# Kernel tuning notes

Hardware: AMD Instinct MI355X
Metric: run time of the kernel (lower is better)

The kernel has to match this reference:

```python
import jax, jax.numpy as jnp
import numpy as np

N_NODES = 50000
N_EDGES = 640000
D_IN = 128
HIDDEN = 128
OUT = 64


def sage_conv(x, edge_index, W_l, b_l, W_r):
    # PyG SAGEConv (mean aggr): out = lin_l(mean_j x_j) + lin_r(x_i)
    src, dst = edge_index[0], edge_index[1]
    msgs = x[src]                                             # [E, d] gather
    agg = jax.ops.segment_sum(msgs, dst, num_segments=x.shape[0])
    cnt = jax.ops.segment_sum(jnp.ones((edge_index.shape[1],), x.dtype), dst,
                              num_segments=x.shape[0])
    mean = agg / jnp.maximum(cnt, 1.0)[:, None]
    return mean @ W_l.T + b_l + x @ W_r.T


def setup_inputs() -> dict:
    key = jax.random.key(0)
    ks = jax.random.split(key, 8)
    s = lambda d: 1.0 / np.sqrt(d)
    x = jax.random.normal(ks[0], (N_NODES, D_IN), dtype=jnp.float32)
    edge_index = jax.random.randint(ks[1], (2, N_EDGES), 0, N_NODES, dtype=jnp.int64)
    return {
        "x": x,
        "edge_index": edge_index,
        "W1_l": jax.random.normal(ks[2], (HIDDEN, D_IN), jnp.float32) * s(D_IN),
        "b1_l": jnp.zeros((HIDDEN,), jnp.float32),
        "W1_r": jax.random.normal(ks[3], (HIDDEN, D_IN), jnp.float32) * s(D_IN),
        "W2_l": jax.random.normal(ks[4], (HIDDEN, HIDDEN), jnp.float32) * s(HIDDEN),
        "b2_l": jnp.zeros((HIDDEN,), jnp.float32),
        "W2_r": jax.random.normal(ks[5], (HIDDEN, HIDDEN), jnp.float32) * s(HIDDEN),
        "W3": jax.random.normal(ks[6], (OUT, HIDDEN), jnp.float32) * s(HIDDEN),
        "b3": jnp.zeros((OUT,), jnp.float32),
    }


def reference(x, edge_index, W1_l, b1_l, W1_r, W2_l, b2_l, W2_r, W3, b3):
    h = jax.nn.relu(sage_conv(x, edge_index, W1_l, b1_l, W1_r))
    h = jax.nn.relu(sage_conv(h, edge_index, W2_l, b2_l, W2_r))
    return h @ W3.T + b3
```

## Files before the change

kernel.cpp:

```cpp
#include <hip/hip_runtime.h>
#include <hip/hip_fp16.h>


typedef _Float16 f16x8 __attribute__((ext_vector_type(8)));
typedef float floatx4 __attribute__((ext_vector_type(4)));
typedef float floatx2 __attribute__((ext_vector_type(2)));

__device__ __forceinline__ unsigned short f2h(float f) {
    __half h = __float2half_rn(f);
    union { __half h; unsigned short s; } c; c.h = h; return c.s;
}
__device__ __forceinline__ __half2 u2h(unsigned u) {
    union { unsigned u; __half2 h; } c; c.u = u; return c.h;
}
__device__ __forceinline__ unsigned h2u(__half2 h) {
    union { __half2 h; unsigned u; } c; c.h = h; return c.u;
}
__device__ __forceinline__ __half2 shx(__half2 v, int m) {
    return u2h((unsigned)__shfl_xor((int)h2u(v), m, 64));
}
__device__ __forceinline__ ushort4 cvt4h(float4 v) {
    ushort4 o;
    o.x = f2h(v.x); o.y = f2h(v.y); o.z = f2h(v.z); o.w = f2h(v.w);
    return o;
}
__device__ __forceinline__ unsigned char f2fp8(float v) {
    return (unsigned char)(__builtin_amdgcn_cvt_pk_fp8_f32(v, v, 0, false) & 0xff);
}

#define ROWU 64
#define SLOTMAX 62
#define WSEG 18432

__global__ __launch_bounds__(256) void prep_kernel(
    const float* __restrict__ W1l, const float* __restrict__ W1r,
    const float* __restrict__ W2l, const float* __restrict__ W2r,
    const float* __restrict__ W3,  const float* __restrict__ x,
    unsigned short* __restrict__ wb,
    unsigned short* __restrict__ xb,
    unsigned char* __restrict__ x8,
    const int* __restrict__ src, const int* __restrict__ dst,
    unsigned short* __restrict__ ell,
    int NX4, int E)
{
    int i = blockIdx.x * 256 + threadIdx.x;
    if (i < E) {
        const int d = dst[i];
        const int s = src[i];
        unsigned short* row = ell + (size_t)d * ROWU;
        const int p = atomicAdd((int*)row, 1);
        if (p < SLOTMAX) row[2 + p] = (unsigned short)s;
        return;
    }
    int j = i - E;
    if (j < WSEG) {
        const float* s; int l;
        if (j < 8192)       { if (j < 4096) { s = W1l; l = j; }
                              else          { s = W1r; l = j - 4096; } }
        else if (j < 16384) { if (j < 12288){ s = W2l; l = j - 8192; }
                              else          { s = W2r; l = j - 12288; } }
        else                { s = W3; l = j - 16384; }
        ((ushort4*)wb)[j] = cvt4h(((const float4*)s)[l]);
        return;
    }
    int k = j - WSEG;
    if (k < NX4) {
        float4 v = ((const float4*)x)[k];
        ((ushort4*)xb)[k] = cvt4h(v);
        unsigned u8 = __builtin_amdgcn_cvt_pk_fp8_f32(v.x, v.y, 0, false);
        u8 = __builtin_amdgcn_cvt_pk_fp8_f32(v.z, v.w, u8, true);
        ((unsigned*)x8)[k] = u8;
    }
}

__global__ __launch_bounds__(256) void agg_kernel(
    const unsigned char* __restrict__ feat8,
    const unsigned short* __restrict__ ell,
    unsigned short* __restrict__ meanG,
    int N)
{
    const int s    = blockIdx.x & 3;
    const int tile = blockIdx.x >> 2;
    const int wave = threadIdx.x >> 6;
    const int lane = threadIdx.x & 63;
    const int g = lane >> 4;
    const int q = (lane >> 2) & 3;
    const int c = lane & 3;

    const int n  = tile * 16 + wave * 4 + q;
    const int nc = (n < N) ? n : 0;
    const int ebase = nc * ROWU;
    int dg = *(const int*)(ell + ebase);
    if (n >= N) dg = 0;
    dg = dg < SLOTMAX ? dg : SLOTMAX;
    const unsigned char* fq = feat8 + s * 32 + c * 8;

    floatx2 a0 = (floatx2)(0.f), a1 = (floatx2)(0.f);
    floatx2 a2 = (floatx2)(0.f), a3 = (floatx2)(0.f);

#pragma unroll
    for (int t = 0; t < 4; ++t) {
        const int j = g + 4 * t;
        const unsigned m = (j < dg) ? 0xffffffffu : 0u;
        int iv = ell[ebase + 2 + (j < dg ? j : 0)];
        iv = iv < N ? iv : 0;
        uint2 p = *(const uint2*)(fq + (size_t)iv * 128);
        p.x &= m; p.y &= m;
        a0 += __builtin_amdgcn_cvt_pk_f32_fp8(p.x, false);
        a1 += __builtin_amdgcn_cvt_pk_f32_fp8(p.x, true);
        a2 += __builtin_amdgcn_cvt_pk_f32_fp8(p.y, false);
        a3 += __builtin_amdgcn_cvt_pk_f32_fp8(p.y, true);
    }
    for (int slot = 16 + g; slot < dg; slot += 4) {
        const int iv = ell[ebase + 2 + slot];
        uint2 p = *(const uint2*)(fq + (size_t)iv * 128);
        a0 += __builtin_amdgcn_cvt_pk_f32_fp8(p.x, false);
        a1 += __builtin_amdgcn_cvt_pk_f32_fp8(p.x, true);
        a2 += __builtin_amdgcn_cvt_pk_f32_fp8(p.y, false);
        a3 += __builtin_amdgcn_cvt_pk_f32_fp8(p.y, true);
    }

    __half2 c0 = __floats2half2_rn(a0.x, a0.y);
    __half2 c1 = __floats2half2_rn(a1.x, a1.y);
    __half2 c2 = __floats2half2_rn(a2.x, a2.y);
    __half2 c3 = __floats2half2_rn(a3.x, a3.y);
    c0 = __hadd2(c0, shx(c0, 16)); c0 = __hadd2(c0, shx(c0, 32));
    c1 = __hadd2(c1, shx(c1, 16)); c1 = __hadd2(c1, shx(c1, 32));
    c2 = __hadd2(c2, shx(c2, 16)); c2 = __hadd2(c2, shx(c2, 32));
    c3 = __hadd2(c3, shx(c3, 16)); c3 = __hadd2(c3, shx(c3, 32));

    if (g == 0 && n < N) {
        const float inv = (dg > 0) ? 1.0f / (float)dg : 0.0f;
        uint4 o;
        o.x = h2u(__floats2half2_rn(__low2float(c0) * inv,
                                    __high2float(c0) * inv));
        o.y = h2u(__floats2half2_rn(__low2float(c1) * inv,
                                    __high2float(c1) * inv));
        o.z = h2u(__floats2half2_rn(__low2float(c2) * inv,
                                    __high2float(c2) * inv));
        o.w = h2u(__floats2half2_rn(__low2float(c3) * inv,
                                    __high2float(c3) * inv));
        *(uint4*)&meanG[(size_t)n * 128 + s * 32 + c * 8] = o;
    }
}

template <bool WFP8, bool HEAD>
__global__ __launch_bounds__(256) void gemm_kernel(
    const unsigned short* __restrict__ feat,
    const unsigned short* __restrict__ meanG,
    const unsigned short* __restrict__ Wl,
    const unsigned short* __restrict__ Wr,
    const float* __restrict__ bias,
    unsigned short* __restrict__ out,
    unsigned char* __restrict__ out8,
    const unsigned short* __restrict__ W3,
    const float* __restrict__ b3,
    float* __restrict__ outF,
    int N, int tiles, int gridB)
{
    __shared__ unsigned short sA[2][16][136];
    __shared__ unsigned short sS[2][16][136];
    __shared__ unsigned short sh2[HEAD ? 16 : 1][136];

    const int tid  = threadIdx.x;
    const int wave = tid >> 6;
    const int lane = tid & 63;
    const int mrow = lane & 15;
    const int quad = lane >> 4;
    const int t0 = wave * 2, t1 = wave * 2 + 1;
    const int srow = tid >> 4;
    const int schk = tid & 15;

    f16x8 wl0[4], wr0[4], wl1[4], wr1[4], w3f[4];
#pragma unroll
    for (int kk = 0; kk < 4; ++kk) {
        const int k = kk * 32 + quad * 8;
        wl0[kk] = *(const f16x8*)(Wl + (size_t)(t0 * 16 + mrow) * 128 + k);
        wr0[kk] = *(const f16x8*)(Wr + (size_t)(t0 * 16 + mrow) * 128 + k);
        wl1[kk] = *(const f16x8*)(Wl + (size_t)(t1 * 16 + mrow) * 128 + k);
        wr1[kk] = *(const f16x8*)(Wr + (size_t)(t1 * 16 + mrow) * 128 + k);
        if (HEAD)
            w3f[kk] = *(const f16x8*)(W3 + (size_t)(wave * 16 + mrow) * 128 + k);
    }
    const float b0 = bias[t0 * 16 + mrow];
    const float b1 = bias[t1 * 16 + mrow];
    const float bh = HEAD ? b3[wave * 16 + mrow] : 0.0f;

    int tile = blockIdx.x;
    bool valid = tile < tiles;
    uint4 pA, pS;
    if (valid) {
        const size_t gb = (size_t)tile * 2048 + srow * 128 + schk * 8;
        pA = *(const uint4*)(meanG + gb);
        pS = *(const uint4*)(feat + gb);
    }
    int buf = 0;

    while (valid) {
        *(uint4*)&sA[buf][srow][schk * 8] = pA;
        *(uint4*)&sS[buf][srow][schk * 8] = pS;
        __syncthreads();

        const int r0 = tile * 16;

        const int ntile = tile + gridB;
        const bool nvalid = ntile < tiles;
        if (nvalid) {
            const size_t gb = (size_t)ntile * 2048 + srow * 128 + schk * 8;
            pA = *(const uint4*)(meanG + gb);
            pS = *(const uint4*)(feat + gb);
        }

        floatx4 acc0 = (floatx4)(0.0f), acc1 = (floatx4)(0.0f);
#pragma unroll
        for (int kk = 0; kk < 4; ++kk) {
            const int k = kk * 32 + quad * 8;
            f16x8 aA = *(const f16x8*)&sA[buf][mrow][k];
            f16x8 aS = *(const f16x8*)&sS[buf][mrow][k];
            acc0 = __builtin_amdgcn_mfma_f32_16x16x32_f16(aA, wl0[kk], acc0, 0, 0, 0);
            acc0 = __builtin_amdgcn_mfma_f32_16x16x32_f16(aS, wr0[kk], acc0, 0, 0, 0);
            acc1 = __builtin_amdgcn_mfma_f32_16x16x32_f16(aA, wl1[kk], acc1, 0, 0, 0);
            acc1 = __builtin_amdgcn_mfma_f32_16x16x32_f16(aS, wr1[kk], acc1, 0, 0, 0);
        }

#pragma unroll
        for (int i = 0; i < 4; ++i) {
            const int r = r0 + quad * 4 + i;
            const float v0 = fmaxf(acc0[i] + b0, 0.0f);
            const float v1 = fmaxf(acc1[i] + b1, 0.0f);
            if (HEAD) {
                sh2[quad * 4 + i][t0 * 16 + mrow] = f2h(v0);
                sh2[quad * 4 + i][t1 * 16 + mrow] = f2h(v1);
            } else if (r < N) {
                out[(size_t)r * 128 + t0 * 16 + mrow] = f2h(v0);
                out[(size_t)r * 128 + t1 * 16 + mrow] = f2h(v1);
                if (WFP8) {
                    out8[(size_t)r * 128 + t0 * 16 + mrow] = f2fp8(v0);
                    out8[(size_t)r * 128 + t1 * 16 + mrow] = f2fp8(v1);
                }
            }
        }

        if (HEAD) {
            __syncthreads();
            floatx4 ah = (floatx4)(0.0f);
#pragma unroll
            for (int kk = 0; kk < 4; ++kk) {
                const int k = kk * 32 + quad * 8;
                f16x8 aA = *(const f16x8*)&sh2[mrow][k];
                ah = __builtin_amdgcn_mfma_f32_16x16x32_f16(aA, w3f[kk], ah, 0, 0, 0);
            }
#pragma unroll
            for (int i = 0; i < 4; ++i) {
                const int r = r0 + quad * 4 + i;
                if (r < N)
                    outF[(size_t)r * 64 + wave * 16 + mrow] = ah[i] + bh;
            }
        }
        buf ^= 1;
        tile = ntile;
        valid = nvalid;
    }
}

extern "C" void kernel_launch(void* const* d_in, const int* in_sizes, int n_in,
                              void* d_out, int out_size, void* d_ws, size_t ws_size,
                              hipStream_t stream)
{
    const float* x   = (const float*)d_in[0];
    const int* ei    = (const int*)d_in[1];
    const float* W1l = (const float*)d_in[2];
    const float* b1l = (const float*)d_in[3];
    const float* W1r = (const float*)d_in[4];
    const float* W2l = (const float*)d_in[5];
    const float* b2l = (const float*)d_in[6];
    const float* W2r = (const float*)d_in[7];
    const float* W3  = (const float*)d_in[8];
    const float* b3  = (const float*)d_in[9];
    float* out = (float*)d_out;

    const int N = in_sizes[0] / 128;
    const int E = in_sizes[1] / 2;
    const int* src = ei;
    const int* dst = ei + E;

    unsigned short* ell  = (unsigned short*)d_ws;
    unsigned short* xb   = ell + (size_t)N * ROWU;
    unsigned short* h1   = xb + (size_t)N * 128;
    unsigned short* mg   = h1 + (size_t)N * 128;
    unsigned short* wb1l = mg + (size_t)N * 128;
    unsigned short* wb1r = wb1l + 16384;
    unsigned short* wb2l = wb1r + 16384;
    unsigned short* wb2r = wb2l + 16384;
    unsigned short* wb3  = wb2r + 16384;
    unsigned char* x8    = (unsigned char*)(wb3 + 8192);
    unsigned char* h18   = x8 + (size_t)N * 128;

    const int tiles = (N + 15) / 16;
    const int NX4   = N * 32;
    const int gemmB = (tiles < 512) ? tiles : 512;

    hipMemsetAsync(ell, 0, (size_t)N * ROWU * 2, stream);
    {
        const int total = E + WSEG + NX4;
        hipLaunchKernelGGL(prep_kernel, dim3((total + 255) / 256), dim3(256), 0,
                           stream, W1l, W1r, W2l, W2r, W3, x, wb1l, xb, x8,
                           src, dst, ell, NX4, E);
    }

    hipLaunchKernelGGL(agg_kernel, dim3(tiles * 4), dim3(256), 0, stream,
                       x8, ell, mg, N);
    hipLaunchKernelGGL((gemm_kernel<true, false>), dim3(gemmB), dim3(256), 0,
                       stream, xb, mg, wb1l, wb1r, b1l,
                       h1, h18, nullptr, nullptr, nullptr, N, tiles, gemmB);

    hipLaunchKernelGGL(agg_kernel, dim3(tiles * 4), dim3(256), 0, stream,
                       h18, ell, mg, N);
    hipLaunchKernelGGL((gemm_kernel<false, true>), dim3(gemmB), dim3(256), 0,
                       stream, h1, mg, wb2l, wb2r, b2l,
                       nullptr, nullptr, wb3, b3, out, N, tiles, gemmB);
}
```

Baseline: 211.7 us.

## Partition ELL edge insertion by XCD so atomics stay in local L2

Edge insertion into the ELL adjacency now runs with 8 blocks per chunk of edges. Each block in a group of 8 handles only the destinations whose low 3 bits match blockIdx&7, which the code treats as the XCD index. Each thread loads 8 edges through vector int4 loads. The goal is to keep the atomics and row writes for a given node on one XCD's L2, avoiding cross-die coherence traffic. In exchange, every edge index is read 8 times and most threads do predicated-off work.

```diff
diff --git a/kernel.cpp b/kernel.cpp
--- a/kernel.cpp
+++ b/kernel.cpp
@@ -31,6 +31,7 @@
 #define ROWU 64
 #define SLOTMAX 62
 #define WSEG 18432
+#define EPT 8
 
 __global__ __launch_bounds__(256) void prep_kernel(
     const float* __restrict__ W1l, const float* __restrict__ W1r,
@@ -41,18 +42,41 @@
     unsigned char* __restrict__ x8,
     const int* __restrict__ src, const int* __restrict__ dst,
     unsigned short* __restrict__ ell,
-    int NX4, int E)
+    int NX4, int E, int EBLK)
 {
-    int i = blockIdx.x * 256 + threadIdx.x;
-    if (i < E) {
-        const int d = dst[i];
-        const int s = src[i];
-        unsigned short* row = ell + (size_t)d * ROWU;
-        const int p = atomicAdd((int*)row, 1);
-        if (p < SLOTMAX) row[2 + p] = (unsigned short)s;
+    if ((int)blockIdx.x < EBLK) {
+        const int xcd   = blockIdx.x & 7;
+        const int chunk = blockIdx.x >> 3;
+        const int base  = (chunk * 256 + threadIdx.x) * EPT;
+        if (base >= E) return;
+        if (base + EPT <= E) {
+            const int4 d0 = ((const int4*)(dst + base))[0];
+            const int4 d1 = ((const int4*)(dst + base))[1];
+            const int4 s0 = ((const int4*)(src + base))[0];
+            const int4 s1 = ((const int4*)(src + base))[1];
+            const int dd[8] = { d0.x, d0.y, d0.z, d0.w, d1.x, d1.y, d1.z, d1.w };
+            const int ss[8] = { s0.x, s0.y, s0.z, s0.w, s1.x, s1.y, s1.z, s1.w };
+#pragma unroll
+            for (int e = 0; e < 8; ++e) {
+                if ((dd[e] & 7) == xcd) {
+                    unsigned short* row = ell + (size_t)dd[e] * ROWU;
+                    const int p = atomicAdd((int*)row, 1);
+                    if (p < SLOTMAX) row[2 + p] = (unsigned short)ss[e];
+                }
+            }
+        } else {
+            for (int e = base; e < E; ++e) {
+                const int d = dst[e];
+                if ((d & 7) == xcd) {
+                    unsigned short* row = ell + (size_t)d * ROWU;
+                    const int p = atomicAdd((int*)row, 1);
+                    if (p < SLOTMAX) row[2 + p] = (unsigned short)src[e];
+                }
+            }
+        }
         return;
     }
-    int j = i - E;
+    int j = ((int)blockIdx.x - EBLK) * 256 + threadIdx.x;
     if (j < WSEG) {
         const float* s; int l;
         if (j < 8192)       { if (j < 4096) { s = W1l; l = j; }
@@ -300,12 +324,15 @@
     const int NX4   = N * 32;
     const int gemmB = (tiles < 512) ? tiles : 512;
 
+    const int nchunks = (E + 256 * EPT - 1) / (256 * EPT);
+    const int EBLK    = nchunks * 8;
+
     hipMemsetAsync(ell, 0, (size_t)N * ROWU * 2, stream);
     {
-        const int total = E + WSEG + NX4;
-        hipLaunchKernelGGL(prep_kernel, dim3((total + 255) / 256), dim3(256), 0,
+        const int cvtB = (WSEG + NX4 + 255) / 256;
+        hipLaunchKernelGGL(prep_kernel, dim3(EBLK + cvtB), dim3(256), 0,
                            stream, W1l, W1r, W2l, W2r, W3, x, wb1l, xb, x8,
-                           src, dst, ell, NX4, E);
+                           src, dst, ell, NX4, E, EBLK);
     }
 
     hipLaunchKernelGGL(agg_kernel, dim3(tiles * 4), dim3(256), 0, stream,
```

New measurement: 246.5 us. 1.16x slower.
